# Kernel optimization log

Hardware: AMD Instinct MI355X
Metric: run time of the kernel (lower is better)

Reference implementation:

```python
import jax, jax.numpy as jnp
import numpy as np

NHEADS = 16


def setup_inputs() -> dict:
    key = jax.random.key(0)
    ks = jax.random.split(key, 5)
    B, S, D = 2, 2048, 1024
    x = jax.random.normal(ks[0], (B, S, D), dtype=jnp.float32)
    W_packed = jax.random.normal(ks[1], (3 * D, D), dtype=jnp.float32) * (1.0 / np.sqrt(D))
    b_packed = jax.random.normal(ks[2], (3 * D,), dtype=jnp.float32) * 0.02
    W_out = jax.random.normal(ks[3], (D, D), dtype=jnp.float32) * (1.0 / np.sqrt(D))
    b_out = jax.random.normal(ks[4], (D,), dtype=jnp.float32) * 0.02
    return {"x": x, "W_packed": W_packed, "b_packed": b_packed, "W_out": W_out, "b_out": b_out}


def reference(x, W_packed, b_packed, W_out, b_out):
    B, S, D = x.shape
    H = NHEADS
    hd = D // H
    # packed QKV projection (self-attention: q is k is v)
    qkv = x @ W_packed.T + b_packed                       # [B,S,3D]
    q, k, v = jnp.split(qkv, 3, axis=-1)

    def heads(t):
        return t.reshape(B, S, H, hd).transpose(0, 2, 1, 3)  # [B,H,S,hd]

    q, k, v = map(heads, (q, k, v))

    # ALiBi slopes per flex path: exp2(-(h+1)*8/H)
    slopes = jnp.exp2(-(jnp.arange(1, H + 1, dtype=x.dtype) * (8.0 / H)))  # [H]
    pos = jnp.arange(S)
    rel = (pos[None, :] - pos[:, None]).astype(x.dtype)    # kv_idx - q_idx, [S,S]
    bias = slopes[:, None, None] * rel                     # [H,S,S]
    causal = pos[None, :] <= pos[:, None]                  # allowed positions
    neg = jnp.finfo(x.dtype).min
    attn_mask = jnp.where(causal[None, :, :], bias, neg)   # [H,S,S]

    scale = 1.0 / np.sqrt(hd)
    scores = jnp.einsum("bhqd,bhkd->bhqk", q, k) * scale + attn_mask[None]
    attn = jax.nn.softmax(scores, axis=-1)
    out = jnp.einsum("bhqk,bhkd->bhqd", attn, v)           # [B,H,S,hd]
    out = out.transpose(0, 2, 1, 3).reshape(B, S, D)
    return out @ W_out.T + b_out
```

## Files before the change

### kernel.cpp

```cpp
#include <hip/hip_runtime.h>

typedef float f32x4 __attribute__((ext_vector_type(4)));
typedef __bf16 bf16x8 __attribute__((ext_vector_type(8)));
typedef unsigned short u16;

__device__ __forceinline__ f32x4 mfma16(bf16x8 a, bf16x8 b, f32x4 c) {
  return __builtin_amdgcn_mfma_f32_16x16x32_bf16(a, b, c, 0, 0, 0);
}

__device__ __forceinline__ int pidx16(int row, int kc) {
  return ((((row >> 6) * 32 + (kc >> 2)) * 4 + ((row >> 4) & 3)) << 6) +
         ((kc & 3) << 4) + (row & 15);
}

__global__ void cvt3_kernel(const float* __restrict__ x,
                            const float* __restrict__ wp,
                            const float* __restrict__ wo,
                            u16* __restrict__ apx, u16* __restrict__ bpx,
                            u16* __restrict__ wox) {
  int idx = blockIdx.x * blockDim.x + threadIdx.x;
  int stride = gridDim.x * blockDim.x;
  for (int i = idx; i < 1048576; i += stride) {
    const float* src;
    u16* dst;
    int j;
    if (i < 524288) {
      j = i; src = x + (size_t)j * 8; dst = apx;
    } else if (i < 917504) {
      j = i - 524288; src = wp + (size_t)j * 8; dst = bpx;
    } else {
      j = i - 917504; src = wo + (size_t)j * 8; dst = wox;
    }
    f32x4 a = *(const f32x4*)src;
    f32x4 b = *(const f32x4*)(src + 4);
    bf16x8 r;
#pragma unroll
    for (int e = 0; e < 4; ++e) {
      r[e] = (__bf16)a[e];
      r[4 + e] = (__bf16)b[e];
    }
    int row = j >> 7, kc = j & 127;
    *(bf16x8*)(dst + (size_t)pidx16(row, kc) * 8) = r;
  }
}

template <int MODE>
__global__ __launch_bounds__(64, 3) void gemm_frag(
    const u16* __restrict__ apx, const u16* __restrict__ bpx,
    const float* __restrict__ bias, float* __restrict__ Cout,
    __bf16* __restrict__ qb, __bf16* __restrict__ kp, __bf16* __restrict__ vp,
    int N, int ntiles) {
  const int lane = threadIdx.x & 63;
  const int lr = lane & 15, lg = lane >> 4;
  const int nwg = gridDim.x;
  const int lid = blockIdx.x;
  const int sw = (lid & 7) * (nwg >> 3) + (lid >> 3);
  const int ni = sw % ntiles, mi = sw / ntiles;

  const u16* ab = apx + (size_t)mi * 65536 + lane * 8;
  const u16* bb = bpx + (size_t)ni * 65536 + lane * 8;

  f32x4 acc[4][4] = {};
  bf16x8 a0[4], b0[4], a1[4], b1[4];
#pragma unroll
  for (int mt = 0; mt < 4; ++mt) {
    a0[mt] = *(const bf16x8*)(ab + mt * 512);
    b0[mt] = *(const bf16x8*)(bb + mt * 512);
  }
  for (int kt = 0; kt < 32; kt += 2) {
#pragma unroll
    for (int mt = 0; mt < 4; ++mt) {
      a1[mt] = *(const bf16x8*)(ab + (kt + 1) * 2048 + mt * 512);
      b1[mt] = *(const bf16x8*)(bb + (kt + 1) * 2048 + mt * 512);
    }
#pragma unroll
    for (int mt = 0; mt < 4; ++mt)
#pragma unroll
      for (int nt = 0; nt < 4; ++nt)
        acc[mt][nt] = mfma16(a0[mt], b0[nt], acc[mt][nt]);
    if (kt + 2 < 32) {
#pragma unroll
      for (int mt = 0; mt < 4; ++mt) {
        a0[mt] = *(const bf16x8*)(ab + (kt + 2) * 2048 + mt * 512);
        b0[mt] = *(const bf16x8*)(bb + (kt + 2) * 2048 + mt * 512);
      }
    }
#pragma unroll
    for (int mt = 0; mt < 4; ++mt)
#pragma unroll
      for (int nt = 0; nt < 4; ++nt)
        acc[mt][nt] = mfma16(a1[mt], b1[nt], acc[mt][nt]);
  }

#pragma unroll
  for (int nt = 0; nt < 4; ++nt) {
    int col = ni * 64 + nt * 16 + lr;
    float bv = bias[col];
#pragma unroll
    for (int mt = 0; mt < 4; ++mt) {
#pragma unroll
      for (int r = 0; r < 4; ++r) {
        int row = mi * 64 + mt * 16 + lg * 4 + r;
        float val = acc[mt][nt][r] + bv;
        if (MODE == 0) {
          Cout[(size_t)row * N + col] = val;
        } else {
          __bf16 bx = (__bf16)val;
          int b = row >> 11, s = row & 2047;
          int third = col >> 10, hd = col & 1023;
          int h = hd >> 6, d = hd & 63;
          if (third == 0) {
            qb[(size_t)row * 1024 + hd] = bx;
          } else {
            int bh = b * 16 + h, t2 = s >> 6, sr = s & 63;
            size_t tb = ((size_t)(bh * 32 + t2)) * 4096;
            if (third == 1)
              kp[tb + (sr >> 4) * 1024 + (d >> 5) * 512 + ((d >> 3) & 3) * 128 +
                 (sr & 15) * 8 + (d & 7)] = bx;
            else
              vp[tb + (d >> 4) * 1024 + (sr >> 5) * 512 + ((sr >> 3) & 3) * 128 +
                 (d & 15) * 8 + (sr & 7)] = bx;
          }
        }
      }
    }
  }
}

__global__ __launch_bounds__(64, 4) void attn_kernel(
    const __bf16* __restrict__ qb, const __bf16* __restrict__ kp,
    const __bf16* __restrict__ vp, u16* __restrict__ abp) {
  __shared__ __bf16 p_lds[16][72];
  const int lane = threadIdx.x & 63;
  const int lr = lane & 15;
  const int lg = lane >> 4;

  const int lid = blockIdx.x;
  const int xcd = lid & 7;
  const int rest = lid >> 3;
  const int bh = xcd * 4 + (rest & 3);
  const int a16 = 127 - (rest >> 2);
  const int b = bh >> 4, h = bh & 15;
  const int qr0 = a16 * 16;
  const int ntl = (a16 >> 2) + 1;

  const float LOG2E = 1.4426950408889634f;
  const float c1 = 0.125f * LOG2E;
  const float c2 = exp2f(-(float)(h + 1) * 0.5f) * LOG2E;

  bf16x8 ones;
#pragma unroll
  for (int j = 0; j < 8; ++j) ones[j] = (__bf16)1.0f;

  const u16* ktiles = (const u16*)kp + (size_t)bh * 32 * 4096;
  const u16* vtiles = (const u16*)vp + (size_t)bh * 32 * 4096;

  const __bf16* qrow = qb + (size_t)(b * 2048 + qr0 + lr) * 1024 + h * 64;
  bf16x8 qf0 = *(const bf16x8*)(qrow + lg * 8);
  bf16x8 qf1 = *(const bf16x8*)(qrow + 32 + lg * 8);

  float m[4], l[4], cq[4];
  f32x4 o[4];
#pragma unroll
  for (int r = 0; r < 4; ++r) {
    m[r] = 0.f;
    l[r] = 0.f;
    cq[r] = c2 * (float)(qr0 + lg * 4 + r);
  }
#pragma unroll
  for (int dt = 0; dt < 4; ++dt) o[dt] = (f32x4){0.f, 0.f, 0.f, 0.f};

  for (int t = 0; t < ntl; ++t) {
    const u16* kb = ktiles + (size_t)t * 4096;
    const u16* vb = vtiles + (size_t)t * 4096;
    const int kv = t * 64;
    const bool last = (t == ntl - 1);

    bf16x8 ka[8], va[8];
#pragma unroll
    for (int j = 0; j < 8; ++j)
      ka[j] = *(const bf16x8*)(kb + j * 512 + lane * 8);
#pragma unroll
    for (int j = 0; j < 8; ++j)
      va[j] = *(const bf16x8*)(vb + j * 512 + lane * 8);

    f32x4 s[4];
#pragma unroll
    for (int nt = 0; nt < 4; ++nt) {
      f32x4 tt = (f32x4){0.f, 0.f, 0.f, 0.f};
      tt = mfma16(qf0, ka[nt * 2], tt);
      tt = mfma16(qf1, ka[nt * 2 + 1], tt);
      s[nt] = tt;
    }

#pragma unroll
    for (int nt = 0; nt < 4; ++nt) {
      float bnt = c2 * (float)(kv + nt * 16 + lr);
#pragma unroll
      for (int r = 0; r < 4; ++r)
        s[nt][r] = __builtin_fmaf(s[nt][r], c1, bnt - cq[r]);
    }
    if (last) {
#pragma unroll
      for (int nt = 0; nt < 4; ++nt) {
        float kf = (float)(kv + nt * 16 + lr);
#pragma unroll
        for (int r = 0; r < 4; ++r) {
          float qi = (float)(qr0 + lg * 4 + r);
          if (kf > qi) s[nt][r] = -1e30f;
        }
      }
    }

    float pm[4];
#pragma unroll
    for (int r = 0; r < 4; ++r)
      pm[r] = fmaxf(fmaxf(s[0][r], s[1][r]), fmaxf(s[2][r], s[3][r]));
    bool ok = (pm[0] <= m[0] + 8.f) && (pm[1] <= m[1] + 8.f) &&
              (pm[2] <= m[2] + 8.f) && (pm[3] <= m[3] + 8.f);
    if (!__all(ok)) {
#pragma unroll
      for (int r = 0; r < 4; ++r)
#pragma unroll
        for (int d = 1; d < 16; d <<= 1)
          pm[r] = fmaxf(pm[r], __shfl_xor(pm[r], d));
#pragma unroll
      for (int r = 0; r < 4; ++r) {
        float mn = fmaxf(m[r], pm[r]);
        float fac = __builtin_amdgcn_exp2f(m[r] - mn);
        m[r] = mn;
        l[r] *= fac;
#pragma unroll
        for (int dt = 0; dt < 4; ++dt) o[dt][r] *= fac;
      }
    }

#pragma unroll
    for (int nt = 0; nt < 4; ++nt)
#pragma unroll
      for (int r = 0; r < 4; ++r) {
        float e = __builtin_amdgcn_exp2f(s[nt][r] - m[r]);
        p_lds[lg * 4 + r][nt * 16 + lr] = (__bf16)e;
      }

    bf16x8 pa0 = *(const bf16x8*)&p_lds[lr][lg * 8];
    bf16x8 pa1 = *(const bf16x8*)&p_lds[lr][32 + lg * 8];

    {
      f32x4 tt = (f32x4){0.f, 0.f, 0.f, 0.f};
      tt = mfma16(pa0, ones, tt);
      tt = mfma16(pa1, ones, tt);
#pragma unroll
      for (int r = 0; r < 4; ++r) l[r] += tt[r];
    }

#pragma unroll
    for (int dt = 0; dt < 4; ++dt) {
      o[dt] = mfma16(pa0, va[dt * 2], o[dt]);
      o[dt] = mfma16(pa1, va[dt * 2 + 1], o[dt]);
    }
  }

  const int mi_g = b * 32 + (a16 >> 2);
#pragma unroll
  for (int dt = 0; dt < 4; ++dt)
#pragma unroll
    for (int r = 0; r < 4; ++r) {
      float val = o[dt][r] / l[r];
      __bf16 bx = (__bf16)val;
      int off16 = (((mi_g * 32 + h * 2 + (dt >> 1)) * 4 + (a16 & 3)) << 6) +
                  (((dt & 1) * 2 + (lr >> 3)) << 4) + lg * 4 + r;
      abp[(size_t)off16 * 8 + (lr & 7)] = *(u16*)&bx;
    }
}

extern "C" void kernel_launch(void* const* d_in, const int* in_sizes, int n_in,
                              void* d_out, int out_size, void* d_ws, size_t ws_size,
                              hipStream_t stream) {
  (void)in_sizes; (void)n_in; (void)out_size; (void)ws_size;
  const float* x = (const float*)d_in[0];
  const float* Wp = (const float*)d_in[1];
  const float* bp = (const float*)d_in[2];
  const float* Wo = (const float*)d_in[3];
  const float* bo = (const float*)d_in[4];
  float* out = (float*)d_out;

  char* ws = (char*)d_ws;
  u16* apx = (u16*)(ws);
  u16* bpx = (u16*)(ws + (size_t)(8u << 20));
  u16* wox = (u16*)(ws + (size_t)(14u << 20));
  u16* qbp = (u16*)(ws + (size_t)(16u << 20));
  u16* kpp = (u16*)(ws + (size_t)(24u << 20));
  u16* vpp = (u16*)(ws + (size_t)(32u << 20));
  u16* abp = (u16*)(ws + (size_t)(40u << 20));

  cvt3_kernel<<<2048, 256, 0, stream>>>(x, Wp, Wo, apx, bpx, wox);
  gemm_frag<1><<<3072, 64, 0, stream>>>(
      apx, bpx, bp, nullptr, (__bf16*)qbp, (__bf16*)kpp, (__bf16*)vpp,
      3072, 48);
  attn_kernel<<<4096, 64, 0, stream>>>(
      (const __bf16*)qbp, (const __bf16*)kpp, (const __bf16*)vpp, abp);
  gemm_frag<0><<<1024, 64, 0, stream>>>(
      abp, wox, bo, out, nullptr, nullptr, nullptr, 1024, 16);
}
```

Before: 123.6 us.

## Group four waves per GEMM workgroup sharing B tile with XCD-aware mapping

Both GEMMs change from one-wave workgroups to 256-thread workgroups. Each wave computes a different 64-row M tile against the same N tile, so B-fragment loads are shared through cache within a workgroup. The block-to-tile mapping now pins M tiles to XCDs for L2 locality. The output projection uses a narrower 32-column N tile to keep enough workgroups, at the cost of less A reuse per MFMA.

Result: faster. 119.6 us (-3.2%).

```diff
diff --git a/kernel.cpp b/kernel.cpp
--- a/kernel.cpp
+++ b/kernel.cpp
@@ -44,63 +44,78 @@
   }
 }
 
-template <int MODE>
-__global__ __launch_bounds__(64, 3) void gemm_frag(
+template <int NREP, int MODE>
+__global__ __launch_bounds__(256, 2) void gemm_frag(
     const u16* __restrict__ apx, const u16* __restrict__ bpx,
     const float* __restrict__ bias, float* __restrict__ Cout,
     __bf16* __restrict__ qb, __bf16* __restrict__ kp, __bf16* __restrict__ vp,
-    int N, int ntiles) {
-  const int lane = threadIdx.x & 63;
+    int N) {
+  const int tid = threadIdx.x;
+  const int wid = tid >> 6;
+  const int lane = tid & 63;
   const int lr = lane & 15, lg = lane >> 4;
-  const int nwg = gridDim.x;
+
   const int lid = blockIdx.x;
-  const int sw = (lid & 7) * (nwg >> 3) + (lid >> 3);
-  const int ni = sw % ntiles, mi = sw / ntiles;
-
-  const u16* ab = apx + (size_t)mi * 65536 + lane * 8;
-  const u16* bb = bpx + (size_t)ni * 65536 + lane * 8;
-
-  f32x4 acc[4][4] = {};
-  bf16x8 a0[4], b0[4], a1[4], b1[4];
-#pragma unroll
-  for (int mt = 0; mt < 4; ++mt) {
-    a0[mt] = *(const bf16x8*)(ab + mt * 512);
-    b0[mt] = *(const bf16x8*)(bb + mt * 512);
-  }
+  const int xcd = lid & 7;
+  const int local = lid >> 3;
+  const int mib = xcd * 2 + (local & 1);
+  const int nj = local >> 1;
+  const int mi64 = mib * 4 + wid;
+
+  const u16* ab = apx + (size_t)mi64 * 65536 + lane * 8;
+  const u16* bb;
+  int colbase;
+  if (NREP == 4) {
+    bb = bpx + (size_t)nj * 65536 + lane * 8;
+    colbase = nj * 64;
+  } else {
+    bb = bpx + (size_t)(nj >> 1) * 65536 + (nj & 1) * 1024 + lane * 8;
+    colbase = nj * 32;
+  }
+
+  f32x4 acc[4][NREP] = {};
+  bf16x8 a0[4], b0[NREP], a1[4], b1[NREP];
+#pragma unroll
+  for (int mt = 0; mt < 4; ++mt) a0[mt] = *(const bf16x8*)(ab + mt * 512);
+#pragma unroll
+  for (int nt = 0; nt < NREP; ++nt) b0[nt] = *(const bf16x8*)(bb + nt * 512);
+
   for (int kt = 0; kt < 32; kt += 2) {
 #pragma unroll
-    for (int mt = 0; mt < 4; ++mt) {
+    for (int mt = 0; mt < 4; ++mt)
       a1[mt] = *(const bf16x8*)(ab + (kt + 1) * 2048 + mt * 512);
-      b1[mt] = *(const bf16x8*)(bb + (kt + 1) * 2048 + mt * 512);
-    }
+#pragma unroll
+    for (int nt = 0; nt < NREP; ++nt)
+      b1[nt] = *(const bf16x8*)(bb + (kt + 1) * 2048 + nt * 512);
 #pragma unroll
     for (int mt = 0; mt < 4; ++mt)
 #pragma unroll
-      for (int nt = 0; nt < 4; ++nt)
+      for (int nt = 0; nt < NREP; ++nt)
         acc[mt][nt] = mfma16(a0[mt], b0[nt], acc[mt][nt]);
     if (kt + 2 < 32) {
 #pragma unroll
-      for (int mt = 0; mt < 4; ++mt) {
+      for (int mt = 0; mt < 4; ++mt)
         a0[mt] = *(const bf16x8*)(ab + (kt + 2) * 2048 + mt * 512);
-        b0[mt] = *(const bf16x8*)(bb + (kt + 2) * 2048 + mt * 512);
-      }
+#pragma unroll
+      for (int nt = 0; nt < NREP; ++nt)
+        b0[nt] = *(const bf16x8*)(bb + (kt + 2) * 2048 + nt * 512);
     }
 #pragma unroll
     for (int mt = 0; mt < 4; ++mt)
 #pragma unroll
-      for (int nt = 0; nt < 4; ++nt)
+      for (int nt = 0; nt < NREP; ++nt)
         acc[mt][nt] = mfma16(a1[mt], b1[nt], acc[mt][nt]);
   }
 
 #pragma unroll
-  for (int nt = 0; nt < 4; ++nt) {
-    int col = ni * 64 + nt * 16 + lr;
+  for (int nt = 0; nt < NREP; ++nt) {
+    int col = colbase + nt * 16 + lr;
     float bv = bias[col];
 #pragma unroll
     for (int mt = 0; mt < 4; ++mt) {
 #pragma unroll
       for (int r = 0; r < 4; ++r) {
-        int row = mi * 64 + mt * 16 + lg * 4 + r;
+        int row = mi64 * 64 + mt * 16 + lg * 4 + r;
         float val = acc[mt][nt][r] + bv;
         if (MODE == 0) {
           Cout[(size_t)row * N + col] = val;
@@ -295,11 +310,10 @@
   u16* abp = (u16*)(ws + (size_t)(40u << 20));
 
   cvt3_kernel<<<2048, 256, 0, stream>>>(x, Wp, Wo, apx, bpx, wox);
-  gemm_frag<1><<<3072, 64, 0, stream>>>(
-      apx, bpx, bp, nullptr, (__bf16*)qbp, (__bf16*)kpp, (__bf16*)vpp,
-      3072, 48);
+  gemm_frag<4, 1><<<768, 256, 0, stream>>>(
+      apx, bpx, bp, nullptr, (__bf16*)qbp, (__bf16*)kpp, (__bf16*)vpp, 3072);
   attn_kernel<<<4096, 64, 0, stream>>>(
       (const __bf16*)qbp, (const __bf16*)kpp, (const __bf16*)vpp, abp);
-  gemm_frag<0><<<1024, 64, 0, stream>>>(
-      abp, wox, bo, out, nullptr, nullptr, nullptr, 1024, 16);
-}
+  gemm_frag<2, 0><<<512, 256, 0, stream>>>(
+      abp, wox, bo, out, nullptr, nullptr, nullptr, 1024);
+}
```
